# Optimization experiments

Measured on AMD Instinct MI355X. Metric: run time of the kernel, lower is better.

Reference implementation:

```python
import jax, jax.numpy as jnp
import numpy as np

EPS = 1e-5

def layer_norm(x, alpha, beta):
    mean = jnp.mean(x, axis=-1, keepdims=True)
    var = jnp.mean(jnp.square(x - mean), axis=-1, keepdims=True)
    return alpha * ((x - mean) / jnp.sqrt(var + EPS)) + beta

def setup_inputs() -> dict:
    key = jax.random.key(0)
    B, S, D, H = 4, 2048, 1024, 16
    Dff = 4 * D
    ks = jax.random.split(key, 8)
    inp = {
        "x": jax.random.normal(ks[0], (B, S, D), jnp.float32),
        "attention_mask": jnp.ones((B, S), jnp.int32),
        "ln1_alpha": jnp.ones((D,), jnp.float32),
        "ln1_beta": jnp.zeros((D,), jnp.float32),
        "ln2_alpha": jnp.ones((D,), jnp.float32),
        "ln2_beta": jnp.zeros((D,), jnp.float32),
        "Wq": jax.random.normal(ks[1], (D, D), jnp.float32) * 0.05,
        "Wk": jax.random.normal(ks[2], (D, D), jnp.float32) * 0.05,
        "Wv": jax.random.normal(ks[3], (D, D), jnp.float32) * 0.05,
        "Wo": jax.random.normal(ks[4], (D, D), jnp.float32) * 0.05,
        "W1": jax.random.normal(ks[5], (D, Dff), jnp.float32) * 0.02,
        "b1": jnp.zeros((Dff,), jnp.float32),
        "W2": jax.random.normal(ks[6], (Dff, D), jnp.float32) * 0.02,
        "b2": jnp.zeros((D,), jnp.float32),
    }
    return inp

def reference(x, attention_mask, ln1_alpha, ln1_beta, ln2_alpha, ln2_beta,
              Wq, Wk, Wv, Wo, W1, b1, W2, b2):
    B, S, D = x.shape
    H = 16
    dh = D // H

    # LN1 + self-attention
    y = layer_norm(x, ln1_alpha, ln1_beta)
    Q = (y @ Wq).reshape(B, S, H, dh).transpose(0, 2, 1, 3)  # [B,H,S,dh]
    K = (y @ Wk).reshape(B, S, H, dh).transpose(0, 2, 1, 3)
    V = (y @ Wv).reshape(B, S, H, dh).transpose(0, 2, 1, 3)

    scores = jnp.einsum("bhqd,bhkd->bhqk", Q, K) / jnp.sqrt(jnp.float32(dh))
    causal = jnp.tril(jnp.ones((S, S), jnp.float32))  # [S,S]
    tmask = attention_mask.astype(jnp.float32)  # [B,S]
    amask = causal[None, None, :, :] * tmask[:, None, None, :] * tmask[:, None, :, None]
    scores = jnp.where(amask > 0, scores, jnp.float32(-1e30))
    attn = jax.nn.softmax(scores, axis=-1)
    # dropout omitted (deterministic inference)
    ctx = jnp.einsum("bhqk,bhkd->bhqd", attn, V)
    ctx = ctx.transpose(0, 2, 1, 3).reshape(B, S, D)
    x = x + ctx @ Wo

    # LN2 + GELU FFN
    y = layer_norm(x, ln2_alpha, ln2_beta)
    h = jax.nn.gelu(y @ W1 + b1, approximate=False)
    x = x + (h @ W2 + b2)
    return x
```

## Files before the change

kernel.cpp:

```cpp
#include <hip/hip_runtime.h>
#include <math.h>

typedef unsigned short u16;
typedef unsigned int u32;
typedef __attribute__((ext_vector_type(4))) unsigned short u16x4;
typedef __attribute__((ext_vector_type(8))) short bf16x8;
typedef __attribute__((ext_vector_type(4))) float f32x4;

#define B_ 4
#define S_ 2048
#define D_ 1024
#define H_ 16
#define NT (B_*S_)
#define DFF 4096

static __device__ __forceinline__ float bf2f(u16 u) {
    return __uint_as_float(((u32)u) << 16);
}
static __device__ __forceinline__ u16 f2bf(float f) {
    u32 u = __float_as_uint(f);
    u32 r = (u + 0x7fffu + ((u >> 16) & 1u)) >> 16;
    return (u16)r;
}
static __device__ __forceinline__ void gload_lds16(const void* g, void* l) {
    __builtin_amdgcn_global_load_lds(
        (const __attribute__((address_space(1))) void*)g,
        (__attribute__((address_space(3))) void*)l, 16, 0, 0);
}
static __device__ __forceinline__ float gelu_fast(float x) {
    float x2 = x * x;
    float u = x * fmaf(0.044715f, x2, 1.0f);
    float e = exp2f(2.3022079f * u);
    float r = __builtin_amdgcn_rcpf(e + 1.0f);
    return x - x * r;
}

#define MBAR() do { asm volatile("" ::: "memory"); \
                    __builtin_amdgcn_s_barrier(); \
                    asm volatile("" ::: "memory"); } while (0)

__global__ void transpose_f2b4(const float* __restrict__ s0, const float* __restrict__ s1,
                               const float* __restrict__ s2, const float* __restrict__ s3,
                               u16* __restrict__ d0, u16* __restrict__ d1,
                               u16* __restrict__ d2, u16* __restrict__ d3,
                               int R, int C) {
    const float* in = s0; u16* out = d0;
    if (blockIdx.z == 1) { in = s1; out = d1; }
    else if (blockIdx.z == 2) { in = s2; out = d2; }
    else if (blockIdx.z == 3) { in = s3; out = d3; }
    __shared__ float t[32][33];
    int c0 = blockIdx.x * 32, r0 = blockIdx.y * 32;
    int x = threadIdx.x, y = threadIdx.y;
    #pragma unroll
    for (int i = 0; i < 4; i++)
        t[y + i*8][x] = in[(long)(r0 + y + i*8) * C + c0 + x];
    __syncthreads();
    #pragma unroll
    for (int i = 0; i < 4; i++)
        out[(long)(c0 + y + i*8) * R + r0 + x] = f2bf(t[x][y + i*8]);
}

__global__ void transpose_f2b(const float* __restrict__ in, u16* __restrict__ out,
                              int R, int C) {
    __shared__ float t[32][33];
    int c0 = blockIdx.x * 32, r0 = blockIdx.y * 32;
    int x = threadIdx.x, y = threadIdx.y;
    #pragma unroll
    for (int i = 0; i < 4; i++)
        t[y + i*8][x] = in[(long)(r0 + y + i*8) * C + c0 + x];
    __syncthreads();
    #pragma unroll
    for (int i = 0; i < 4; i++)
        out[(long)(c0 + y + i*8) * R + r0 + x] = f2bf(t[x][y + i*8]);
}

__global__ void transpose_v(const u16* __restrict__ V, u16* __restrict__ Vt) {
    __shared__ u16 t[32][33];
    int z = blockIdx.z; int b = z >> 4, h = z & 15;
    int s0 = blockIdx.x * 32, d0 = blockIdx.y * 32;
    int x = threadIdx.x, y = threadIdx.y;
    const u16* in = V + ((long)b * S_ + s0) * D_ + h * 64 + d0;
    #pragma unroll
    for (int i = 0; i < 4; i++)
        t[y + i*8][x] = in[(long)(y + i*8) * D_ + x];
    __syncthreads();
    u16* out = Vt + ((long)z * 64 + d0) * S_ + s0;
    #pragma unroll
    for (int i = 0; i < 4; i++)
        out[(long)(y + i*8) * S_ + x] = t[x][y + i*8];
}

__global__ __launch_bounds__(256) void ln_kernel(
    const float* __restrict__ X, const float* __restrict__ alpha,
    const float* __restrict__ beta, u16* __restrict__ Y) {
    int row = blockIdx.x, tid = threadIdx.x;
    float4 xv = ((const float4*)(X + (long)row * D_))[tid];
    float v[4] = {xv.x, xv.y, xv.z, xv.w};
    float s = 0.f, ss = 0.f;
    #pragma unroll
    for (int i = 0; i < 4; i++) { s += v[i]; ss += v[i]*v[i]; }
    #pragma unroll
    for (int off = 32; off >= 1; off >>= 1) {
        s += __shfl_xor(s, off);
        ss += __shfl_xor(ss, off);
    }
    __shared__ float red[8];
    __shared__ float stats[2];
    int w = tid >> 6;
    if ((tid & 63) == 0) { red[w] = s; red[4 + w] = ss; }
    __syncthreads();
    if (tid == 0) {
        float S = red[0] + red[1] + red[2] + red[3];
        float SS = red[4] + red[5] + red[6] + red[7];
        float mean = S * (1.f / D_);
        float var = SS * (1.f / D_) - mean * mean;
        stats[0] = mean; stats[1] = rsqrtf(var + 1e-5f);
    }
    __syncthreads();
    float mean = stats[0], rstd = stats[1];
    float4 av = ((const float4*)alpha)[tid];
    float4 bv = ((const float4*)beta)[tid];
    u16x4 o;
    o[0] = f2bf((v[0] - mean) * rstd * av.x + bv.x);
    o[1] = f2bf((v[1] - mean) * rstd * av.y + bv.y);
    o[2] = f2bf((v[2] - mean) * rstd * av.z + bv.z);
    o[3] = f2bf((v[3] - mean) * rstd * av.w + bv.w);
    *(u16x4*)(Y + (long)row * D_ + tid * 4) = o;
}

#define BM 128
#define BN 128
#define BK 64

__global__ __launch_bounds__(256, 3) void gemm_bt(
    const u16* __restrict__ A,
    const u16* __restrict__ Bt0, const u16* __restrict__ Bt1, const u16* __restrict__ Bt2,
    void* __restrict__ C0, void* __restrict__ C1, void* __restrict__ C2,
    int M, int N, int K, int mode,
    const float* __restrict__ bias, const float* __restrict__ resid) {
    const u16* Bt = Bt0; void* C = C0;
    if (blockIdx.z == 1) { Bt = Bt1; C = C1; }
    else if (blockIdx.z == 2) { Bt = Bt2; C = C2; }

    __shared__ __align__(16) u16 Asm[BM * BK];
    __shared__ __align__(16) u16 Bsm[BN * BK];

    int tid = threadIdx.x;
    int lane = tid & 63, wave = tid >> 6;
    int l15 = lane & 15, quad = lane >> 4;
    int wm = wave & 1, wn = wave >> 1;
    long tm0 = (long)blockIdx.y * BM, tn0 = (long)blockIdx.x * BN;

    int srow = lane >> 3;
    int scol = (lane & 7) * 8;

    f32x4 acc[4][4] = {};

    for (int k0 = 0; k0 < K; k0 += BK) {
        __syncthreads();
        #pragma unroll
        for (int c = 0; c < 4; c++) {
            int chunk = wave * 4 + c;
            int row = chunk * 8 + srow;
            gload_lds16(&A[(tm0 + row) * (long)K + k0 + scol], &Asm[chunk * 512]);
            gload_lds16(&Bt[(tn0 + row) * (long)K + k0 + scol], &Bsm[chunk * 512]);
        }
        __syncthreads();
        #pragma unroll
        for (int ks = 0; ks < 2; ks++) {
            bf16x8 af[4], bfm[4];
            #pragma unroll
            for (int mt = 0; mt < 4; mt++)
                af[mt] = *(const bf16x8*)&Asm[(wm*64 + mt*16 + l15) * BK + ks*32 + quad*8];
            #pragma unroll
            for (int nt = 0; nt < 4; nt++)
                bfm[nt] = *(const bf16x8*)&Bsm[(wn*64 + nt*16 + l15) * BK + ks*32 + quad*8];
            #pragma unroll
            for (int mt = 0; mt < 4; mt++)
                #pragma unroll
                for (int nt = 0; nt < 4; nt++)
                    acc[mt][nt] = __builtin_amdgcn_mfma_f32_16x16x32_bf16(
                        af[mt], bfm[nt], acc[mt][nt], 0, 0, 0);
        }
    }

    #pragma unroll
    for (int mt = 0; mt < 4; mt++) {
        #pragma unroll
        for (int nt = 0; nt < 4; nt++) {
            #pragma unroll
            for (int i = 0; i < 4; i++) {
                long r = tm0 + wm*64 + mt*16 + quad*4 + i;
                long cn = tn0 + wn*64 + nt*16 + l15;
                long idx = r * N + cn;
                float val = acc[mt][nt][i];
                if (mode == 0) {
                    ((u16*)C)[idx] = f2bf(val);
                } else if (mode == 1) {
                    ((float*)C)[idx] = val + resid[idx];
                } else if (mode == 2) {
                    val += bias[cn];
                    ((u16*)C)[idx] = f2bf(gelu_fast(val));
                } else {
                    ((float*)C)[idx] = val + bias[cn] + resid[idx];
                }
            }
        }
    }
}

#define BM2 256
#define BN2 256
#define BK2 64

__global__ __launch_bounds__(512, 2) void gemm8p(
    const u16* __restrict__ A, const u16* __restrict__ Bt,
    u16* __restrict__ C0, u16* __restrict__ C1, u16* __restrict__ C2,
    int N, int K, int mode, const float* __restrict__ bias) {
    __shared__ __align__(16) u16 lds[2 * 32768];

    int tid = threadIdx.x;
    int lane = tid & 63, wave = tid >> 6;
    int l15 = lane & 15, quad = lane >> 4;
    int wm = wave & 1, wn = wave >> 1;
    long tm0 = (long)blockIdx.y * BM2, tn0 = (long)blockIdx.x * BN2;
    int srow = lane >> 3;
    int scol = (lane & 7) * 8;
    int steps = K >> 6;

    auto STAGE = [&](int kt, int half, int buf) {
        long kk = (long)kt * BK2;
        #pragma unroll
        for (int c = 0; c < 2; c++) {
            int chunk = wave * 2 + c;
            int rloc = (half & 1) * 128 + chunk * 8 + srow;
            const u16* g = (half < 2)
                ? &A [(tm0 + rloc) * (long)K + kk + scol]
                : &Bt[(tn0 + rloc) * (long)K + kk + scol];
            u16* l = &lds[buf * 32768 + (half >= 2 ? 16384 : 0)
                          + (half & 1) * 8192 + chunk * 512];
            gload_lds16(g, l);
        }
    };

    f32x4 acc[8][4] = {};
    bf16x8 af[4][2], bl[2][2], bh[2][2];

    STAGE(0, 0, 0); STAGE(0, 1, 0); STAGE(0, 2, 0); STAGE(0, 3, 0);
    if (steps > 1) { STAGE(1, 2, 1); STAGE(1, 3, 1); }
    if (steps > 1) asm volatile("s_waitcnt vmcnt(4)" ::: "memory");
    else           asm volatile("s_waitcnt vmcnt(0)" ::: "memory");
    MBAR();

    for (int t = 0; t < steps; ++t) {
        int cur = t & 1;
        const u16* Ab = &lds[cur * 32768];
        const u16* Bb = &lds[cur * 32768 + 16384];
        bool pf1 = (t + 1 < steps), pf2 = (t + 2 < steps);

        #pragma unroll
        for (int mt = 0; mt < 4; mt++) {
            const u16* p = &Ab[(wm*128 + mt*16 + l15) * BK2];
            af[mt][0] = *(const bf16x8*)(p + quad*8);
            af[mt][1] = *(const bf16x8*)(p + 32 + quad*8);
        }
        #pragma unroll
        for (int nt = 0; nt < 2; nt++) {
            const u16* p = &Bb[(wn*64 + nt*16 + l15) * BK2];
            bl[nt][0] = *(const bf16x8*)(p + quad*8);
            bl[nt][1] = *(const bf16x8*)(p + 32 + quad*8);
        }
        if (pf1) STAGE(t + 1, 0, cur ^ 1);
        MBAR();
        __builtin_amdgcn_s_setprio(1);
        #pragma unroll
        for (int mt = 0; mt < 4; mt++)
            #pragma unroll
            for (int nt = 0; nt < 2; nt++) {
                acc[mt][nt] = __builtin_amdgcn_mfma_f32_16x16x32_bf16(af[mt][0], bl[nt][0], acc[mt][nt], 0,0,0);
                acc[mt][nt] = __builtin_amdgcn_mfma_f32_16x16x32_bf16(af[mt][1], bl[nt][1], acc[mt][nt], 0,0,0);
            }
        __builtin_amdgcn_s_setprio(0);
        MBAR();

        #pragma unroll
        for (int nt = 0; nt < 2; nt++) {
            const u16* p = &Bb[(wn*64 + (2+nt)*16 + l15) * BK2];
            bh[nt][0] = *(const bf16x8*)(p + quad*8);
            bh[nt][1] = *(const bf16x8*)(p + 32 + quad*8);
        }
        if (pf1) STAGE(t + 1, 1, cur ^ 1);
        MBAR();
        __builtin_amdgcn_s_setprio(1);
        #pragma unroll
        for (int mt = 0; mt < 4; mt++)
            #pragma unroll
            for (int nt = 0; nt < 2; nt++) {
                acc[mt][2+nt] = __builtin_amdgcn_mfma_f32_16x16x32_bf16(af[mt][0], bh[nt][0], acc[mt][2+nt], 0,0,0);
                acc[mt][2+nt] = __builtin_amdgcn_mfma_f32_16x16x32_bf16(af[mt][1], bh[nt][1], acc[mt][2+nt], 0,0,0);
            }
        __builtin_amdgcn_s_setprio(0);
        MBAR();

        #pragma unroll
        for (int mt = 0; mt < 4; mt++) {
            const u16* p = &Ab[(wm*128 + 64 + mt*16 + l15) * BK2];
            af[mt][0] = *(const bf16x8*)(p + quad*8);
            af[mt][1] = *(const bf16x8*)(p + 32 + quad*8);
        }
        if (pf2) STAGE(t + 2, 2, cur);
        MBAR();
        __builtin_amdgcn_s_setprio(1);
        #pragma unroll
        for (int mt = 0; mt < 4; mt++)
            #pragma unroll
            for (int nt = 0; nt < 2; nt++) {
                acc[4+mt][2+nt] = __builtin_amdgcn_mfma_f32_16x16x32_bf16(af[mt][0], bh[nt][0], acc[4+mt][2+nt], 0,0,0);
                acc[4+mt][2+nt] = __builtin_amdgcn_mfma_f32_16x16x32_bf16(af[mt][1], bh[nt][1], acc[4+mt][2+nt], 0,0,0);
            }
        __builtin_amdgcn_s_setprio(0);
        MBAR();

        if (pf2) STAGE(t + 2, 3, cur);
        MBAR();
        __builtin_amdgcn_s_setprio(1);
        #pragma unroll
        for (int mt = 0; mt < 4; mt++)
            #pragma unroll
            for (int nt = 0; nt < 2; nt++) {
                acc[4+mt][nt] = __builtin_amdgcn_mfma_f32_16x16x32_bf16(af[mt][0], bl[nt][0], acc[4+mt][nt], 0,0,0);
                acc[4+mt][nt] = __builtin_amdgcn_mfma_f32_16x16x32_bf16(af[mt][1], bl[nt][1], acc[4+mt][nt], 0,0,0);
            }
        __builtin_amdgcn_s_setprio(0);
        if (pf2) asm volatile("s_waitcnt vmcnt(4)" ::: "memory");
        else     asm volatile("s_waitcnt vmcnt(0)" ::: "memory");
        MBAR();
    }

    #pragma unroll
    for (int mt = 0; mt < 8; mt++) {
        #pragma unroll
        for (int nt = 0; nt < 4; nt++) {
            #pragma unroll
            for (int i = 0; i < 4; i++) {
                long r = tm0 + wm*128 + mt*16 + quad*4 + i;
                int cn = (int)tn0 + wn*64 + nt*16 + l15;
                float val = acc[mt][nt][i];
                if (mode == 0) {
                    int mi = cn >> 10;
                    int col = cn & 1023;
                    u16* base = (mi == 0) ? C0 : (mi == 1 ? C1 : C2);
                    base[r * 1024 + col] = f2bf(val);
                } else {
                    val += bias[cn];
                    C0[r * (long)N + cn] = f2bf(gelu_fast(val));
                }
            }
        }
    }
}

#define LDP 72

__global__ __launch_bounds__(256, 2) void attn_kernel(
    const u16* __restrict__ Q, const u16* __restrict__ Kg, const u16* __restrict__ Vt,
    const int* __restrict__ mask, u16* __restrict__ O) {
    __shared__ __align__(16) u16 Psm[4][32 * LDP];
    int tid = threadIdx.x;
    int lane = tid & 63, wave = tid >> 6;
    int l15 = lane & 15, quad = lane >> 4;
    int bh = blockIdx.x; int b = bh >> 4, h = bh & 15;
    int y = blockIdx.y;
    long tokBase = (long)b * S_;
    const float SCL = 0.125f * 1.4426950408889634f;
    const float MMAX = 20.0f;

    const bf16x8 ones = {16256,16256,16256,16256,16256,16256,16256,16256};
    u16* Pw = Psm[wave];
    const int* mb = mask + b * S_;

    int t;
    if (wave == 0)      t = y;
    else if (wave == 1) t = 63 - y;
    else if (wave == 2) t = 31 - y;
    else                t = 32 + y;
    int q0 = t * 32;

    bf16x8 aq[2][2];
    #pragma unroll
    for (int mt = 0; mt < 2; mt++) {
        const u16* qptr = Q + (tokBase + q0 + mt*16 + l15) * D_ + h * 64;
        aq[mt][0] = *(const bf16x8*)(qptr + quad * 8);
        aq[mt][1] = *(const bf16x8*)(qptr + 32 + quad * 8);
    }

    f32x4 o[2][4] = {};
    f32x4 lacc[2] = {};
    int ktiles = t / 2 + 1;

    for (int kt = 0; kt < ktiles; kt++) {
        int k0 = kt * 64;
        bf16x8 kb[4][2], vb[4][2];
        #pragma unroll
        for (int nt = 0; nt < 4; nt++) {
            const u16* kp = Kg + (tokBase + k0 + nt*16 + l15) * D_ + h * 64;
            kb[nt][0] = *(const bf16x8*)(kp + quad * 8);
            kb[nt][1] = *(const bf16x8*)(kp + 32 + quad * 8);
        }
        #pragma unroll
        for (int d = 0; d < 4; d++) {
            const u16* vp = Vt + ((long)bh * 64 + d*16 + l15) * S_ + k0;
            vb[d][0] = *(const bf16x8*)(vp + quad * 8);
            vb[d][1] = *(const bf16x8*)(vp + 32 + quad * 8);
        }

        f32x4 s[2][4] = {};
        #pragma unroll
        for (int nt = 0; nt < 4; nt++) {
            s[0][nt] = __builtin_amdgcn_mfma_f32_16x16x32_bf16(aq[0][0], kb[nt][0], s[0][nt], 0,0,0);
            s[0][nt] = __builtin_amdgcn_mfma_f32_16x16x32_bf16(aq[0][1], kb[nt][1], s[0][nt], 0,0,0);
            s[1][nt] = __builtin_amdgcn_mfma_f32_16x16x32_bf16(aq[1][0], kb[nt][0], s[1][nt], 0,0,0);
            s[1][nt] = __builtin_amdgcn_mfma_f32_16x16x32_bf16(aq[1][1], kb[nt][1], s[1][nt], 0,0,0);
        }

        int mk = 0;
        #pragma unroll
        for (int nt = 0; nt < 4; nt++)
            if (mb[k0 + nt*16 + l15] != 0) mk |= (1 << nt);

        #pragma unroll
        for (int mt = 0; mt < 2; mt++) {
            #pragma unroll
            for (int i = 0; i < 4; i++) {
                int qq = q0 + mt*16 + quad*4 + i;
                #pragma unroll
                for (int nt = 0; nt < 4; nt++) {
                    int kc = k0 + nt*16 + l15;
                    float p = exp2f(fmaf(s[mt][nt][i], SCL, -MMAX));
                    p = (kc <= qq && ((mk >> nt) & 1)) ? p : 0.f;
                    Pw[(mt*16 + quad*4 + i) * LDP + nt*16 + l15] = f2bf(p);
                }
            }
        }
        asm volatile("s_waitcnt lgkmcnt(0)" ::: "memory");

        #pragma unroll
        for (int hv = 0; hv < 2; hv++) {
            bf16x8 ap0 = *(const bf16x8*)&Pw[l15 * LDP + hv*32 + quad*8];
            bf16x8 ap1 = *(const bf16x8*)&Pw[(16 + l15) * LDP + hv*32 + quad*8];
            #pragma unroll
            for (int d = 0; d < 4; d++) {
                o[0][d] = __builtin_amdgcn_mfma_f32_16x16x32_bf16(ap0, vb[d][hv], o[0][d], 0,0,0);
                o[1][d] = __builtin_amdgcn_mfma_f32_16x16x32_bf16(ap1, vb[d][hv], o[1][d], 0,0,0);
            }
            lacc[0] = __builtin_amdgcn_mfma_f32_16x16x32_bf16(ap0, ones, lacc[0], 0,0,0);
            lacc[1] = __builtin_amdgcn_mfma_f32_16x16x32_bf16(ap1, ones, lacc[1], 0,0,0);
        }
    }

    #pragma unroll
    for (int mt = 0; mt < 2; mt++) {
        #pragma unroll
        for (int i = 0; i < 4; i++) {
            float inv = 1.f / lacc[mt][i];
            long r = tokBase + q0 + mt*16 + quad*4 + i;
            #pragma unroll
            for (int d = 0; d < 4; d++)
                O[r * D_ + h*64 + d*16 + l15] = f2bf(o[mt][d][i] * inv);
        }
    }
}

extern "C" void kernel_launch(void* const* d_in, const int* in_sizes, int n_in,
                              void* d_out, int out_size, void* d_ws, size_t ws_size,
                              hipStream_t stream) {
    const float* x    = (const float*)d_in[0];
    const int*   am   = (const int*)d_in[1];
    const float* ln1a = (const float*)d_in[2];
    const float* ln1b = (const float*)d_in[3];
    const float* ln2a = (const float*)d_in[4];
    const float* ln2b = (const float*)d_in[5];
    const float* wq   = (const float*)d_in[6];
    const float* wk   = (const float*)d_in[7];
    const float* wv   = (const float*)d_in[8];
    const float* wo   = (const float*)d_in[9];
    const float* w1   = (const float*)d_in[10];
    const float* b1   = (const float*)d_in[11];
    const float* w2   = (const float*)d_in[12];
    const float* b2   = (const float*)d_in[13];
    float* out = (float*)d_out;

    char* ws = (char*)d_ws;
    const size_t MB16 = (size_t)16 * 1024 * 1024;
    u16* y1      = (u16*)(ws + 0 * MB16);
    u16* q       = (u16*)(ws + 1 * MB16);
    u16* k       = (u16*)(ws + 2 * MB16);
    u16* v       = (u16*)(ws + 3 * MB16);
    u16* wqt     = (u16*)(ws + 4 * MB16 + 0 * (size_t)D_ * D_ * 2);
    u16* wkt     = (u16*)(ws + 4 * MB16 + 1 * (size_t)D_ * D_ * 2);
    u16* wvt     = (u16*)(ws + 4 * MB16 + 2 * (size_t)D_ * D_ * 2);
    u16* wot     = (u16*)(ws + 4 * MB16 + 3 * (size_t)D_ * D_ * 2);
    u16* y2      = y1;
    u16* w1t     = q;
    u16* w2t     = q + (size_t)D_ * DFF;
    u16* h_full  = k;
    u16* ctx     = v;
    u16*   vt  = (u16*)d_out;
    float* x1f = out;

    dim3 tb(32, 8);
    transpose_f2b4<<<dim3(D_/32, D_/32, 4), tb, 0, stream>>>(
        wq, wk, wv, wo, wqt, wkt, wvt, wot, D_, D_);

    ln_kernel<<<NT, 256, 0, stream>>>(x, ln1a, ln1b, y1);

    gemm8p<<<dim3(3*D_/BN2, NT/BM2), 512, 0, stream>>>(
        y1, wqt, q, k, v, 3*D_, D_, 0, nullptr);

    transpose_v<<<dim3(S_/32, 2, B_*H_), tb, 0, stream>>>(v, vt);

    attn_kernel<<<dim3(B_*H_, 16), 256, 0, stream>>>(q, k, vt, am, ctx);

    gemm_bt<<<dim3(D_/BN, NT/BM, 1), 256, 0, stream>>>(
        ctx, wot, wot, wot, x1f, x1f, x1f, NT, D_, D_, 1, nullptr, x);

    transpose_f2b<<<dim3(DFF/32, D_/32), tb, 0, stream>>>(w1, w1t, D_, DFF);
    transpose_f2b<<<dim3(D_/32, DFF/32), tb, 0, stream>>>(w2, w2t, DFF, D_);

    ln_kernel<<<NT, 256, 0, stream>>>(x1f, ln2a, ln2b, y2);

    gemm8p<<<dim3(DFF/BN2, NT/BM2), 512, 0, stream>>>(
        y2, w1t, h_full, h_full, h_full, DFF, D_, 2, b1);
    gemm_bt<<<dim3(D_/BN, NT/BM, 1), 256, 0, stream>>>(
        h_full, w2t, w2t, w2t, out, out, out, NT, D_, DFF, 3, b2, x1f);
}
```

Baseline: 676.3 us.

## Swizzle GEMM LDS layout and prefetch next K tile in attention

The GEMM's global-to-LDS staging now XOR-swizzles the 16-byte column chunk by row, and the fragment reads apply the matching XOR. This is meant to remove LDS bank conflicts when lanes read rows spaced 64 elements apart. In the attention kernel, the K fragments for the next key tile are loaded into registers before the softmax and PV work of the current tile. That hides global-load latency at the cost of extra VGPRs, which may lower occupancy.

```diff
diff --git a/kernel.cpp b/kernel.cpp
--- a/kernel.cpp
+++ b/kernel.cpp
@@ -225,7 +225,10 @@
     int wm = wave & 1, wn = wave >> 1;
     long tm0 = (long)blockIdx.y * BM2, tn0 = (long)blockIdx.x * BN2;
     int srow = lane >> 3;
-    int scol = (lane & 7) * 8;
+    int scolw = ((lane & 7) ^ srow) * 8;
+    int sk = l15 & 7;
+    int ca0 = ((quad) ^ sk) * 8;
+    int ca1 = ((4 + quad) ^ sk) * 8;
     int steps = K >> 6;
 
     auto STAGE = [&](int kt, int half, int buf) {
@@ -235,8 +238,8 @@
             int chunk = wave * 2 + c;
             int rloc = (half & 1) * 128 + chunk * 8 + srow;
             const u16* g = (half < 2)
-                ? &A [(tm0 + rloc) * (long)K + kk + scol]
-                : &Bt[(tn0 + rloc) * (long)K + kk + scol];
+                ? &A [(tm0 + rloc) * (long)K + kk + scolw]
+                : &Bt[(tn0 + rloc) * (long)K + kk + scolw];
             u16* l = &lds[buf * 32768 + (half >= 2 ? 16384 : 0)
                           + (half & 1) * 8192 + chunk * 512];
             gload_lds16(g, l);
@@ -260,15 +263,15 @@
 
         #pragma unroll
         for (int mt = 0; mt < 4; mt++) {
-            const u16* p = &Ab[(wm*128 + mt*16 + l15) * BK2];
-            af[mt][0] = *(const bf16x8*)(p + quad*8);
-            af[mt][1] = *(const bf16x8*)(p + 32 + quad*8);
+            int row = wm*128 + mt*16 + l15;
+            af[mt][0] = *(const bf16x8*)&Ab[row * BK2 + ca0];
+            af[mt][1] = *(const bf16x8*)&Ab[row * BK2 + ca1];
         }
         #pragma unroll
         for (int nt = 0; nt < 2; nt++) {
-            const u16* p = &Bb[(wn*64 + nt*16 + l15) * BK2];
-            bl[nt][0] = *(const bf16x8*)(p + quad*8);
-            bl[nt][1] = *(const bf16x8*)(p + 32 + quad*8);
+            int row = wn*64 + nt*16 + l15;
+            bl[nt][0] = *(const bf16x8*)&Bb[row * BK2 + ca0];
+            bl[nt][1] = *(const bf16x8*)&Bb[row * BK2 + ca1];
         }
         if (pf1) STAGE(t + 1, 0, cur ^ 1);
         MBAR();
@@ -285,9 +288,9 @@
 
         #pragma unroll
         for (int nt = 0; nt < 2; nt++) {
-            const u16* p = &Bb[(wn*64 + (2+nt)*16 + l15) * BK2];
-            bh[nt][0] = *(const bf16x8*)(p + quad*8);
-            bh[nt][1] = *(const bf16x8*)(p + 32 + quad*8);
+            int row = wn*64 + (2+nt)*16 + l15;
+            bh[nt][0] = *(const bf16x8*)&Bb[row * BK2 + ca0];
+            bh[nt][1] = *(const bf16x8*)&Bb[row * BK2 + ca1];
         }
         if (pf1) STAGE(t + 1, 1, cur ^ 1);
         MBAR();
@@ -304,9 +307,9 @@
 
         #pragma unroll
         for (int mt = 0; mt < 4; mt++) {
-            const u16* p = &Ab[(wm*128 + 64 + mt*16 + l15) * BK2];
-            af[mt][0] = *(const bf16x8*)(p + quad*8);
-            af[mt][1] = *(const bf16x8*)(p + 32 + quad*8);
+            int row = wm*128 + 64 + mt*16 + l15;
+            af[mt][0] = *(const bf16x8*)&Ab[row * BK2 + ca0];
+            af[mt][1] = *(const bf16x8*)&Ab[row * BK2 + ca1];
         }
         if (pf2) STAGE(t + 2, 2, cur);
         MBAR();
@@ -398,15 +401,17 @@
     f32x4 lacc[2] = {};
     int ktiles = t / 2 + 1;
 
+    bf16x8 kb[4][2];
+    #pragma unroll
+    for (int nt = 0; nt < 4; nt++) {
+        const u16* kp = Kg + (tokBase + nt*16 + l15) * D_ + h * 64;
+        kb[nt][0] = *(const bf16x8*)(kp + quad * 8);
+        kb[nt][1] = *(const bf16x8*)(kp + 32 + quad * 8);
+    }
+
     for (int kt = 0; kt < ktiles; kt++) {
         int k0 = kt * 64;
-        bf16x8 kb[4][2], vb[4][2];
-        #pragma unroll
-        for (int nt = 0; nt < 4; nt++) {
-            const u16* kp = Kg + (tokBase + k0 + nt*16 + l15) * D_ + h * 64;
-            kb[nt][0] = *(const bf16x8*)(kp + quad * 8);
-            kb[nt][1] = *(const bf16x8*)(kp + 32 + quad * 8);
-        }
+        bf16x8 vb[4][2];
         #pragma unroll
         for (int d = 0; d < 4; d++) {
             const u16* vp = Vt + ((long)bh * 64 + d*16 + l15) * S_ + k0;
@@ -421,6 +426,15 @@
             s[0][nt] = __builtin_amdgcn_mfma_f32_16x16x32_bf16(aq[0][1], kb[nt][1], s[0][nt], 0,0,0);
             s[1][nt] = __builtin_amdgcn_mfma_f32_16x16x32_bf16(aq[1][0], kb[nt][0], s[1][nt], 0,0,0);
             s[1][nt] = __builtin_amdgcn_mfma_f32_16x16x32_bf16(aq[1][1], kb[nt][1], s[1][nt], 0,0,0);
+        }
+
+        int k1 = (kt + 1 < ktiles) ? k0 + 64 : k0;
+        bf16x8 kbn[4][2];
+        #pragma unroll
+        for (int nt = 0; nt < 4; nt++) {
+            const u16* kp = Kg + (tokBase + k1 + nt*16 + l15) * D_ + h * 64;
+            kbn[nt][0] = *(const bf16x8*)(kp + quad * 8);
+            kbn[nt][1] = *(const bf16x8*)(kp + 32 + quad * 8);
         }
 
         int mk = 0;
@@ -455,6 +469,12 @@
             }
             lacc[0] = __builtin_amdgcn_mfma_f32_16x16x32_bf16(ap0, ones, lacc[0], 0,0,0);
             lacc[1] = __builtin_amdgcn_mfma_f32_16x16x32_bf16(ap1, ones, lacc[1], 0,0,0);
+        }
+
+        #pragma unroll
+        for (int nt = 0; nt < 4; nt++) {
+            kb[nt][0] = kbn[nt][0];
+            kb[nt][1] = kbn[nt][1];
         }
     }
 
```

After: 633.3 us. 6.4% less time.
